# Performance work log

Hardware: AMD Instinct MI355X
Metric: run time of the kernel (lower is better)

The kernel has to match this reference:

```python
import jax, jax.numpy as jnp
import numpy as np

N_NODES = 100000
N_EDGES = 500000
IN_DIM, HID, N_CLS = 128, 512, 40


def gcn_conv(x, W, b, src, dst, num_nodes):
    # PyG GCNConv: h = x W; add self-loops; norm = d^-1/2[src] * d^-1/2[dst];
    # out[dst] += norm * h[src]; out += bias
    h = x @ W  # [N, out_dim]
    ones = jnp.ones(src.shape[0], dtype=x.dtype)
    deg = jax.ops.segment_sum(ones, dst, num_segments=num_nodes)  # in-degree incl self-loops
    dinv = jnp.where(deg > 0, jax.lax.rsqrt(deg), 0.0)
    norm = dinv[src] * dinv[dst]  # [E]
    msgs = h[src] * norm[:, None]  # [E, out_dim] gather + scale
    out = jax.ops.segment_sum(msgs, dst, num_segments=num_nodes)
    return out + b


def setup_inputs() -> dict:
    key = jax.random.key(0)
    k1, k2, k3, k4, k5, k6 = jax.random.split(key, 6)
    x = jax.random.normal(k1, (N_NODES, IN_DIM), dtype=jnp.float32)
    edge_index = jax.random.randint(k2, (2, N_EDGES), 0, N_NODES, dtype=jnp.int32)
    # Glorot-ish params
    W1 = jax.random.normal(k3, (IN_DIM, HID), dtype=jnp.float32) * (1.0 / np.sqrt(IN_DIM))
    b1 = jnp.zeros((HID,), dtype=jnp.float32)
    W2 = jax.random.normal(k4, (HID, N_CLS), dtype=jnp.float32) * (1.0 / np.sqrt(HID))
    b2 = jnp.zeros((N_CLS,), dtype=jnp.float32)
    return {"x": x, "edge_index": edge_index, "W1": W1, "b1": b1, "W2": W2, "b2": b2}


def reference(x, edge_index, W1, b1, W2, b2):
    n = x.shape[0]
    # add self-loops once, shared by both conv layers
    loop = jnp.arange(n, dtype=edge_index.dtype)
    src = jnp.concatenate([edge_index[0], loop])
    dst = jnp.concatenate([edge_index[1], loop])
    h = gcn_conv(x, W1, b1, src, dst, n)
    h = jax.nn.relu(h)
    # dropout is identity in eval mode (reference computed in eval)
    h = gcn_conv(h, W2, b2, src, dst, n)
    return jax.nn.log_softmax(h, axis=1)
```

## Files before the change

### kernel.cpp

```cpp
#include <hip/hip_runtime.h>
#include <cstdint>
#include <cstddef>

#define N_NODES 100000
#define N_EDGES 500000
#define IN_DIM  128
#define HID     512
#define N_CLS   40
#define N_SBLK  ((N_NODES + 255) / 256)
#define N_CNTB  ((N_EDGES + 255) / 256)
#define N_XBFB  12500
#define N_G1B   12500
#define N_PREPB 352

typedef short bf16x8 __attribute__((ext_vector_type(8)));
typedef float f32x4 __attribute__((ext_vector_type(4)));

__device__ inline unsigned short f2bf(float f) {
  unsigned u = __float_as_uint(f);
  u = u + 0x7fffu + ((u >> 16) & 1u);
  return (unsigned short)(u >> 16);
}
__device__ inline float blo(unsigned u) { return __uint_as_float(u << 16); }
__device__ inline float bhi(unsigned u) { return __uint_as_float(u & 0xffff0000u); }

__global__ __launch_bounds__(256) void k_zero(int* __restrict__ cnt, unsigned* __restrict__ flags) {
  int i = blockIdx.x * 256 + threadIdx.x;
  if (i < N_NODES) cnt[i] = 0;
  if (i == 0) flags[0] = 0;
}

__global__ __launch_bounds__(256) void k_count(const int* __restrict__ dst, int* __restrict__ cnt,
                                               int* __restrict__ rank) {
  int e = blockIdx.x * 256 + threadIdx.x;
  if (e < N_EDGES) rank[e] = atomicAdd(&cnt[dst[e]], 1);
}

__global__ __launch_bounds__(256) void k_scan(const int* __restrict__ cnt, unsigned* __restrict__ flags,
                                              int* __restrict__ offsets, float* __restrict__ dinv) {
  __shared__ int s[256];
  __shared__ int base_sh;
  int b = blockIdx.x;
  int i = b * 256 + threadIdx.x;
  int v = (i < N_NODES) ? cnt[i] : 0;
  s[threadIdx.x] = v;
  __syncthreads();
  #pragma unroll
  for (int off = 1; off < 256; off <<= 1) {
    int t = (threadIdx.x >= off) ? s[threadIdx.x - off] : 0;
    __syncthreads();
    s[threadIdx.x] += t;
    __syncthreads();
  }
  int incl = s[threadIdx.x];
  if (threadIdx.x == 0)
    base_sh = (int)atomicAdd(&flags[0], (unsigned)s[255]);
  __syncthreads();
  if (i < N_NODES) {
    int excl = base_sh + incl - v;
    offsets[i] = excl;
    dinv[i]    = rsqrtf((float)(v + 1));
  }
}

__global__ __launch_bounds__(256) void k_fill_xbf(const int* __restrict__ src, const int* __restrict__ dst,
                                                  const int* __restrict__ rank, const int* __restrict__ offsets,
                                                  const float* __restrict__ dinv, int2* __restrict__ epair,
                                                  const float* __restrict__ x, uint2* __restrict__ xb2) {
  int b = blockIdx.x;
  if (b < N_CNTB) {
    int e = b * 256 + threadIdx.x;
    if (e >= N_EDGES) return;
    int s = src[e], d = dst[e];
    int pos = offsets[d] + rank[e];
    float nrm = dinv[s] * dinv[d];
    epair[pos] = make_int2(s, __float_as_int(nrm));
  } else {
    int t = (b - N_CNTB) * 256 + threadIdx.x;
    float4 v = ((const float4*)x)[t];
    uint2 o;
    o.x = (unsigned)f2bf(v.x) | ((unsigned)f2bf(v.y) << 16);
    o.y = (unsigned)f2bf(v.z) | ((unsigned)f2bf(v.w) << 16);
    xb2[t] = o;
  }
}

__global__ __launch_bounds__(256) void k_gather1(const uint2* __restrict__ xb, const int2* __restrict__ ep,
                                                 const int* __restrict__ offsets, const int* __restrict__ cnt,
                                                 const float* __restrict__ dinv, uint2* __restrict__ z1,
                                                 const float* __restrict__ W1, const float* __restrict__ W2,
                                                 unsigned short* __restrict__ W1F, unsigned short* __restrict__ W2F) {
  int b = blockIdx.x;
  if (b >= N_G1B) {
    int t = (b - N_G1B) * 256 + threadIdx.x;
    if (t < 65536) {
      int j = t & 7, lane = (t >> 3) & 63, rest = t >> 9;
      int s2 = rest & 3, c = rest >> 2;
      int k = s2 * 32 + (lane >> 4) * 8 + j;
      int n = c * 16 + (lane & 15);
      W1F[t] = f2bf(W1[k * HID + n]);
    } else {
      int u = t - 65536;
      int j = u & 7, lane = (u >> 3) & 63, rest = u >> 9;
      int ct = rest % 3, gk = rest / 3;
      int k = gk * 32 + (lane >> 4) * 8 + j;
      int col = ct * 16 + (lane & 15);
      W2F[u] = (col < N_CLS) ? f2bf(W2[k * N_CLS + col]) : (unsigned short)0;
    }
    return;
  }
  int lane = threadIdx.x & 63, h = lane >> 5, l = lane & 31;
  int d = b * 8 + (threadIdx.x >> 6) * 2 + h;
  int start = offsets[d], end = start + cnt[d];
  float dd = dinv[d], sl = dd * dd;
  uint2 su = xb[(size_t)d * 32 + l];
  float a0 = sl * blo(su.x), a1 = sl * bhi(su.x), a2 = sl * blo(su.y), a3 = sl * bhi(su.y);
  float p0a = 0.f, p1a = 0.f, p2a = 0.f, p3a = 0.f;
  float q0a = 0.f, q1a = 0.f, q2a = 0.f, q3a = 0.f;
  float r0a = 0.f, r1a = 0.f, r2a = 0.f, r3a = 0.f;

  int i = start;
  for (; i + 3 < end; i += 4) {
    int2 e0 = ep[i], e1 = ep[i + 1], e2 = ep[i + 2], e3 = ep[i + 3];
    uint2 r0 = xb[(size_t)e0.x * 32 + l];
    uint2 r1 = xb[(size_t)e1.x * 32 + l];
    uint2 r2 = xb[(size_t)e2.x * 32 + l];
    uint2 r3 = xb[(size_t)e3.x * 32 + l];
    float n0 = __int_as_float(e0.y), n1 = __int_as_float(e1.y);
    float n2 = __int_as_float(e2.y), n3 = __int_as_float(e3.y);
    a0  += n0 * blo(r0.x); a1  += n0 * bhi(r0.x); a2  += n0 * blo(r0.y); a3  += n0 * bhi(r0.y);
    p0a += n1 * blo(r1.x); p1a += n1 * bhi(r1.x); p2a += n1 * blo(r1.y); p3a += n1 * bhi(r1.y);
    q0a += n2 * blo(r2.x); q1a += n2 * bhi(r2.x); q2a += n2 * blo(r2.y); q3a += n2 * bhi(r2.y);
    r0a += n3 * blo(r3.x); r1a += n3 * bhi(r3.x); r2a += n3 * blo(r3.y); r3a += n3 * bhi(r3.y);
  }
  for (; i < end; ++i) {
    int2 e0 = ep[i];
    uint2 r0 = xb[(size_t)e0.x * 32 + l];
    float n0 = __int_as_float(e0.y);
    a0 += n0 * blo(r0.x); a1 += n0 * bhi(r0.x); a2 += n0 * blo(r0.y); a3 += n0 * bhi(r0.y);
  }
  a0 += p0a + q0a + r0a;
  a1 += p1a + q1a + r1a;
  a2 += p2a + q2a + r2a;
  a3 += p3a + q3a + r3a;
  uint2 o;
  o.x = (unsigned)f2bf(a0) | ((unsigned)f2bf(a1) << 16);
  o.y = (unsigned)f2bf(a2) | ((unsigned)f2bf(a3) << 16);
  z1[(size_t)d * 32 + l] = o;
}

#define HS_STRIDE 56
__global__ __launch_bounds__(64) void k_fused_mfma(const unsigned short* __restrict__ z1b,
                                                   const unsigned short* __restrict__ W1F,
                                                   const float* __restrict__ b1,
                                                   const unsigned short* __restrict__ W2F,
                                                   unsigned short* __restrict__ Pb) {
  __shared__ unsigned short Hs[64 * HS_STRIDE];
  const int lane = threadIdx.x;
  const int c16  = lane & 15, quad = lane >> 4;
  const int odd  = c16 & 1;
  const int mbase = blockIdx.x * 64;

  bf16x8 afrag[4][4];
  #pragma unroll
  for (int t = 0; t < 4; ++t) {
    int mrow = mbase + t * 16 + c16;
    int meff = (mrow < N_NODES) ? mrow : 0;
    const bf16x8* arow = (const bf16x8*)(z1b + (size_t)meff * IN_DIM + quad * 8);
    afrag[t][0] = arow[0];
    afrag[t][1] = arow[4];
    afrag[t][2] = arow[8];
    afrag[t][3] = arow[12];
  }

  f32x4 pacc[4][3];
  #pragma unroll
  for (int t = 0; t < 4; ++t)
    #pragma unroll
    for (int ct = 0; ct < 3; ++ct) pacc[t][ct] = (f32x4){0.f, 0.f, 0.f, 0.f};

  const bf16x8* w1f = (const bf16x8*)W1F;
  const bf16x8* w2f = (const bf16x8*)W2F;
  unsigned short* hs = Hs;

  for (int g = 0; g < 16; ++g) {
    #pragma unroll
    for (int nt = 0; nt < 2; ++nt) {
      int c = g * 2 + nt;
      bf16x8 bp0 = w1f[(c * 4 + 0) * 64 + lane];
      bf16x8 bp1 = w1f[(c * 4 + 1) * 64 + lane];
      bf16x8 bp2 = w1f[(c * 4 + 2) * 64 + lane];
      bf16x8 bp3 = w1f[(c * 4 + 3) * 64 + lane];
      f32x4 h[4];
      #pragma unroll
      for (int t = 0; t < 4; ++t) h[t] = (f32x4){0.f, 0.f, 0.f, 0.f};
      #pragma unroll
      for (int t = 0; t < 4; ++t) h[t] = __builtin_amdgcn_mfma_f32_16x16x32_bf16(afrag[t][0], bp0, h[t], 0, 0, 0);
      #pragma unroll
      for (int t = 0; t < 4; ++t) h[t] = __builtin_amdgcn_mfma_f32_16x16x32_bf16(afrag[t][1], bp1, h[t], 0, 0, 0);
      #pragma unroll
      for (int t = 0; t < 4; ++t) h[t] = __builtin_amdgcn_mfma_f32_16x16x32_bf16(afrag[t][2], bp2, h[t], 0, 0, 0);
      #pragma unroll
      for (int t = 0; t < 4; ++t) h[t] = __builtin_amdgcn_mfma_f32_16x16x32_bf16(afrag[t][3], bp3, h[t], 0, 0, 0);
      float bias = b1[c * 16 + c16];
      int colb = nt * 16 + (c16 & ~1);
      int rb0  = quad * 4 + (odd ? 2 : 0);
      #pragma unroll
      for (int t = 0; t < 4; ++t) {
        float v0 = fmaxf(h[t][0] + bias, 0.f);
        float v1 = fmaxf(h[t][1] + bias, 0.f);
        float v2 = fmaxf(h[t][2] + bias, 0.f);
        float v3 = fmaxf(h[t][3] + bias, 0.f);
        float o0 = __shfl_xor(v0, 1, 64);
        float o1 = __shfl_xor(v1, 1, 64);
        float o2 = __shfl_xor(v2, 1, 64);
        float o3 = __shfl_xor(v3, 1, 64);
        float lo0 = odd ? o2 : v0, hi0 = odd ? v2 : o0;
        float lo1 = odd ? o3 : v1, hi1 = odd ? v3 : o1;
        unsigned p0, p1;
        asm("v_cvt_pk_bf16_f32 %0, %1, %2" : "=v"(p0) : "v"(lo0), "v"(hi0));
        asm("v_cvt_pk_bf16_f32 %0, %1, %2" : "=v"(p1) : "v"(lo1), "v"(hi1));
        *(unsigned*)(hs + (t * 16 + rb0    ) * HS_STRIDE + colb) = p0;
        *(unsigned*)(hs + (t * 16 + rb0 + 1) * HS_STRIDE + colb) = p1;
      }
    }
    bf16x8 hf[4];
    #pragma unroll
    for (int t = 0; t < 4; ++t)
      hf[t] = *(const bf16x8*)(hs + (t * 16 + c16) * HS_STRIDE + quad * 8);
    #pragma unroll
    for (int ct = 0; ct < 3; ++ct) {
      bf16x8 bf = w2f[(g * 3 + ct) * 64 + lane];
      #pragma unroll
      for (int t = 0; t < 4; ++t)
        pacc[t][ct] = __builtin_amdgcn_mfma_f32_16x16x32_bf16(hf[t], bf, pacc[t][ct], 0, 0, 0);
    }
  }

  #pragma unroll
  for (int t = 0; t < 4; ++t) {
    int mrow0 = mbase + t * 16 + quad * 4;
    #pragma unroll
    for (int ct = 0; ct < 3; ++ct) {
      int col = ct * 16 + c16;
      if (col < N_CLS) {
        #pragma unroll
        for (int r = 0; r < 4; ++r) {
          int m = mrow0 + r;
          if (m < N_NODES) Pb[(size_t)m * N_CLS + col] = f2bf(pacc[t][ct][r]);
        }
      }
    }
  }
}

__global__ __launch_bounds__(256) void k_gather2_lsm(const uint2* __restrict__ Pu2,
                                                     const int2* __restrict__ ep,
                                                     const int* __restrict__ offsets, const int* __restrict__ cnt,
                                                     const float* __restrict__ dinv, const float* __restrict__ b2,
                                                     float* __restrict__ out) {
  int lane = threadIdx.x & 63, q = lane >> 4, l = lane & 15;
  int d = blockIdx.x * 16 + (threadIdx.x >> 6) * 4 + q;
  bool act = l < 10;
  int lc = act ? l : 0;
  int start = offsets[d], end = start + cnt[d];
  float dd = dinv[d], sl = dd * dd;

  uint2 su = Pu2[(size_t)d * 10 + lc];
  float a0 = sl * blo(su.x), a1 = sl * bhi(su.x), a2 = sl * blo(su.y), a3 = sl * bhi(su.y);
  float p0a = 0.f, p1a = 0.f, p2a = 0.f, p3a = 0.f;
  float q0a = 0.f, q1a = 0.f, q2a = 0.f, q3a = 0.f;
  float r0a = 0.f, r1a = 0.f, r2a = 0.f, r3a = 0.f;

  int i = start;
  for (; i + 3 < end; i += 4) {
    int2 e0 = ep[i], e1 = ep[i + 1], e2 = ep[i + 2], e3 = ep[i + 3];
    uint2 u0 = Pu2[(size_t)e0.x * 10 + lc];
    uint2 u1 = Pu2[(size_t)e1.x * 10 + lc];
    uint2 u2 = Pu2[(size_t)e2.x * 10 + lc];
    uint2 u3 = Pu2[(size_t)e3.x * 10 + lc];
    float n0 = __int_as_float(e0.y), n1 = __int_as_float(e1.y);
    float n2 = __int_as_float(e2.y), n3 = __int_as_float(e3.y);
    a0  += n0 * blo(u0.x); a1  += n0 * bhi(u0.x); a2  += n0 * blo(u0.y); a3  += n0 * bhi(u0.y);
    p0a += n1 * blo(u1.x); p1a += n1 * bhi(u1.x); p2a += n1 * blo(u1.y); p3a += n1 * bhi(u1.y);
    q0a += n2 * blo(u2.x); q1a += n2 * bhi(u2.x); q2a += n2 * blo(u2.y); q3a += n2 * bhi(u2.y);
    r0a += n3 * blo(u3.x); r1a += n3 * bhi(u3.x); r2a += n3 * blo(u3.y); r3a += n3 * bhi(u3.y);
  }
  for (; i < end; ++i) {
    int2 e0 = ep[i];
    uint2 u0 = Pu2[(size_t)e0.x * 10 + lc];
    float n0 = __int_as_float(e0.y);
    a0 += n0 * blo(u0.x); a1 += n0 * bhi(u0.x); a2 += n0 * blo(u0.y); a3 += n0 * bhi(u0.y);
  }

  float v0, v1, v2, v3;
  if (act) {
    float4 bb = ((const float4*)b2)[l];
    v0 = a0 + p0a + q0a + r0a + bb.x;
    v1 = a1 + p1a + q1a + r1a + bb.y;
    v2 = a2 + p2a + q2a + r2a + bb.z;
    v3 = a3 + p3a + q3a + r3a + bb.w;
  } else {
    v0 = v1 = v2 = v3 = -1e30f;
  }
  float m = fmaxf(fmaxf(v0, v1), fmaxf(v2, v3));
  #pragma unroll
  for (int off = 8; off > 0; off >>= 1) m = fmaxf(m, __shfl_xor(m, off, 64));
  float e = act ? (expf(v0 - m) + expf(v1 - m) + expf(v2 - m) + expf(v3 - m)) : 0.f;
  float s = e;
  #pragma unroll
  for (int off = 8; off > 0; off >>= 1) s += __shfl_xor(s, off, 64);
  float lse = m + logf(s);
  if (act) {
    float4 o = make_float4(v0 - lse, v1 - lse, v2 - lse, v3 - lse);
    ((float4*)(out + (size_t)d * N_CLS))[l] = o;
  }
}

extern "C" void kernel_launch(void* const* d_in, const int* in_sizes, int n_in,
                              void* d_out, int out_size, void* d_ws, size_t ws_size,
                              hipStream_t stream) {
  const float* x  = (const float*)d_in[0];
  const int*   ei = (const int*)d_in[1];
  const int*  src = ei;
  const int*  dst = ei + N_EDGES;
  const float* W1 = (const float*)d_in[2];
  const float* b1 = (const float*)d_in[3];
  const float* W2 = (const float*)d_in[4];
  const float* b2 = (const float*)d_in[5];
  float* out = (float*)d_out;

  float* dinv    = (float*)d_ws;
  int*   cnt     = (int*)(dinv + 131072);
  int*   offsets = cnt + 131072;
  unsigned* flags = (unsigned*)(offsets + 131072);
  int*   rank    = (int*)(flags + 1024);
  int2*  epair   = (int2*)(rank + 524288);
  uint2* xb2     = (uint2*)(epair + 524288);
  unsigned short* Pb = (unsigned short*)xb2;
  unsigned short* z1b = (unsigned short*)(xb2 + 3200000);
  unsigned short* W1F = z1b + (size_t)N_NODES * IN_DIM;
  unsigned short* W2F = W1F + HID * IN_DIM;

  k_zero    <<<N_SBLK, 256, 0, stream>>>(cnt, flags);
  k_count   <<<N_CNTB, 256, 0, stream>>>(dst, cnt, rank);
  k_scan    <<<N_SBLK, 256, 0, stream>>>(cnt, flags, offsets, dinv);
  k_fill_xbf<<<N_CNTB + N_XBFB, 256, 0, stream>>>(src, dst, rank, offsets, dinv, epair, x, xb2);
  k_gather1 <<<N_G1B + N_PREPB, 256, 0, stream>>>(xb2, epair, offsets, cnt, dinv, (uint2*)z1b,
                                                  W1, W2, W1F, W2F);
  k_fused_mfma<<<(N_NODES + 63) / 64, 64, 0, stream>>>(z1b, W1F, b1, W2F, Pb);
  k_gather2_lsm<<<N_NODES / 16, 256, 0, stream>>>((const uint2*)Pb, epair, offsets, cnt, dinv, b2, out);
}
```

Before: 226.9 us.

## Share W1/W2 fragments across four waves via double-buffered LDS staging

The fused MFMA kernel now runs four waves per block, each handling 64 rows. The per-group W1 and W2 fragments are loaded cooperatively into double-buffered shared memory, with the next group prefetched into registers during compute. Previously every 64-thread block read the weight fragments straight from global/L2. This cuts redundant weight traffic by four, at the cost of added __syncthreads barriers, more LDS use and fewer blocks.

```diff
diff --git a/kernel.cpp b/kernel.cpp
--- a/kernel.cpp
+++ b/kernel.cpp
@@ -150,16 +150,18 @@
 }
 
 #define HS_STRIDE 56
-__global__ __launch_bounds__(64) void k_fused_mfma(const unsigned short* __restrict__ z1b,
-                                                   const unsigned short* __restrict__ W1F,
-                                                   const float* __restrict__ b1,
-                                                   const unsigned short* __restrict__ W2F,
-                                                   unsigned short* __restrict__ Pb) {
-  __shared__ unsigned short Hs[64 * HS_STRIDE];
-  const int lane = threadIdx.x;
+__global__ __launch_bounds__(256) void k_fused_mfma(const unsigned short* __restrict__ z1b,
+                                                    const unsigned short* __restrict__ W1F,
+                                                    const float* __restrict__ b1,
+                                                    const unsigned short* __restrict__ W2F,
+                                                    unsigned short* __restrict__ Pb) {
+  __shared__ unsigned short Hs[4][64 * HS_STRIDE];
+  __shared__ uint4 Bs[2][704];
+  const int tid  = threadIdx.x;
+  const int w    = tid >> 6, lane = tid & 63;
   const int c16  = lane & 15, quad = lane >> 4;
   const int odd  = c16 & 1;
-  const int mbase = blockIdx.x * 64;
+  const int mbase = blockIdx.x * 256 + w * 64;
 
   bf16x8 afrag[4][4];
   #pragma unroll
@@ -179,18 +181,35 @@
     #pragma unroll
     for (int ct = 0; ct < 3; ++ct) pacc[t][ct] = (f32x4){0.f, 0.f, 0.f, 0.f};
 
-  const bf16x8* w1f = (const bf16x8*)W1F;
-  const bf16x8* w2f = (const bf16x8*)W2F;
-  unsigned short* hs = Hs;
+  const uint4* w1g = (const uint4*)W1F;
+  const uint4* w2g = (const uint4*)W2F;
+  unsigned short* hs = Hs[w];
+  const int t2 = (tid < 192) ? tid : 191;
+
+  Bs[0][tid]       = w1g[tid];
+  Bs[0][tid + 256] = w1g[256 + tid];
+  if (tid < 192) Bs[0][512 + tid] = w2g[t2];
+  __syncthreads();
 
   for (int g = 0; g < 16; ++g) {
+    const int cur = g & 1;
+    uint4 s0, s1, s2;
+    if (g < 15) {
+      int gn = g + 1;
+      s0 = w1g[gn * 512 + tid];
+      s1 = w1g[gn * 512 + 256 + tid];
+      s2 = w2g[gn * 192 + t2];
+    }
+    const bf16x8* b1f = (const bf16x8*)(&Bs[cur][0]);
+    const bf16x8* b2f = (const bf16x8*)(&Bs[cur][512]);
+
     #pragma unroll
     for (int nt = 0; nt < 2; ++nt) {
       int c = g * 2 + nt;
-      bf16x8 bp0 = w1f[(c * 4 + 0) * 64 + lane];
-      bf16x8 bp1 = w1f[(c * 4 + 1) * 64 + lane];
-      bf16x8 bp2 = w1f[(c * 4 + 2) * 64 + lane];
-      bf16x8 bp3 = w1f[(c * 4 + 3) * 64 + lane];
+      bf16x8 bp0 = b1f[(nt * 4 + 0) * 64 + lane];
+      bf16x8 bp1 = b1f[(nt * 4 + 1) * 64 + lane];
+      bf16x8 bp2 = b1f[(nt * 4 + 2) * 64 + lane];
+      bf16x8 bp3 = b1f[(nt * 4 + 3) * 64 + lane];
       f32x4 h[4];
       #pragma unroll
       for (int t = 0; t < 4; ++t) h[t] = (f32x4){0.f, 0.f, 0.f, 0.f};
@@ -230,10 +249,17 @@
       hf[t] = *(const bf16x8*)(hs + (t * 16 + c16) * HS_STRIDE + quad * 8);
     #pragma unroll
     for (int ct = 0; ct < 3; ++ct) {
-      bf16x8 bf = w2f[(g * 3 + ct) * 64 + lane];
+      bf16x8 bf = b2f[ct * 64 + lane];
       #pragma unroll
       for (int t = 0; t < 4; ++t)
         pacc[t][ct] = __builtin_amdgcn_mfma_f32_16x16x32_bf16(hf[t], bf, pacc[t][ct], 0, 0, 0);
+    }
+    if (g < 15) {
+      const int nb = cur ^ 1;
+      Bs[nb][tid]       = s0;
+      Bs[nb][tid + 256] = s1;
+      if (tid < 192) Bs[nb][512 + tid] = s2;
+      __syncthreads();
     }
   }
 
@@ -348,6 +374,6 @@
   k_fill_xbf<<<N_CNTB + N_XBFB, 256, 0, stream>>>(src, dst, rank, offsets, dinv, epair, x, xb2);
   k_gather1 <<<N_G1B + N_PREPB, 256, 0, stream>>>(xb2, epair, offsets, cnt, dinv, (uint2*)z1b,
                                                   W1, W2, W1F, W2F);
-  k_fused_mfma<<<(N_NODES + 63) / 64, 64, 0, stream>>>(z1b, W1F, b1, W2F, Pb);
+  k_fused_mfma<<<(N_NODES + 255) / 256, 256, 0, stream>>>(z1b, W1F, b1, W2F, Pb);
   k_gather2_lsm<<<N_NODES / 16, 256, 0, stream>>>((const uint2*)Pb, epair, offsets, cnt, dinv, b2, out);
 }
```

After: 231.0 us. No clear change (+1.8%).
